# Kernel tuning notes

Hardware: AMD Instinct MI355X
Metric: run time of the kernel (lower is better)

Reference implementation:

```python
import jax, jax.numpy as jnp
import numpy as np
import math

D = 512      # d_model = sd_dim*2
DFF = 512    # dim_feedforward
S = 512      # num_seg (queries)
T = 32768    # video frames (keys)
RATE = 4     # self-attention band half-width
SCALE = 1.0 / math.sqrt(D)


def _ln(x, g, b):
    m = x.mean(-1, keepdims=True)
    v = ((x - m) ** 2).mean(-1, keepdims=True)
    return (x - m) / jnp.sqrt(v + 1e-5) * g + b


def setup_inputs() -> dict:
    key = jax.random.key(0)
    ks = jax.random.split(key, 12)
    w = lambda k, shp, s=0.02: jax.random.normal(k, shp, jnp.float32) * s
    # exactly S contiguous action segments over T frames
    action_idx = jnp.asarray((np.arange(T) * S) // T, dtype=jnp.int32)
    return dict(
        tgt=w(ks[0], (S, 1, D), 1.0), memory=w(ks[1], (T, 1, D), 1.0),
        pos=w(ks[2], (T, 1, D), 0.1), query_pos=w(ks[3], (S, 1, D), 0.1),
        action_idx=action_idx,
        ca_t2l_w=w(ks[4], (D, D)), ca_t2l_b=jnp.zeros(D),
        ca_l1_w=w(ks[5], (DFF, D)), ca_l1_b=jnp.zeros(DFF),
        ca_l2_w=w(ks[6], (D, DFF)), ca_l2_b=jnp.zeros(D),
        ca_n2_g=jnp.ones(D), ca_n2_b=jnp.zeros(D),
        ca_n3_g=jnp.ones(D), ca_n3_b=jnp.zeros(D),
        sa_conv_w=w(ks[7], (D, D)), sa_conv_b=jnp.zeros(D),
        sa_l1_w=w(ks[8], (DFF, D)), sa_l1_b=jnp.zeros(DFF),
        sa_l2_w=w(ks[9], (D, DFF)), sa_l2_b=jnp.zeros(D),
        sa_n1_g=jnp.ones(D), sa_n1_b=jnp.zeros(D),
        sa_n2_g=jnp.ones(D), sa_n2_b=jnp.zeros(D),
    )


def reference(tgt, memory, pos, query_pos, action_idx,
              ca_t2l_w, ca_t2l_b, ca_l1_w, ca_l1_b, ca_l2_w, ca_l2_b,
              ca_n2_g, ca_n2_b, ca_n3_g, ca_n3_b,
              sa_conv_w, sa_conv_b, sa_l1_w, sa_l1_b, sa_l2_w, sa_l2_b,
              sa_n1_g, sa_n1_b, sa_n2_g, sa_n2_b):
    # ---------------- CrossAttention (segment mask) ----------------
    q = tgt + query_pos                      # (S,1,D)
    k = memory + pos                         # (T,1,D)
    scores = jnp.einsum('sbd,tbd->bst', q, k) * SCALE   # (1,S,T)
    # segment id per frame from change points of action_idx
    chg = (action_idx[1:] != action_idx[:-1]).astype(jnp.int32)
    seg_id = jnp.concatenate([jnp.zeros(1, jnp.int32), jnp.cumsum(chg)])  # (T,)
    # query i attends to segments i-1, i, i+1
    mask = jnp.abs(seg_id[None, :] - jnp.arange(S, dtype=jnp.int32)[:, None]) <= 1  # (S,T)
    scores = jnp.where(mask[None], scores, -jnp.inf)
    attn = jax.nn.softmax(scores, axis=-1)               # (1,S,T)
    tgt2 = jnp.einsum('bst,tbd->sbd', attn, memory)      # (S,1,D)
    tgt2 = jnp.maximum(tgt2, 0.0) @ ca_t2l_w.T + ca_t2l_b
    x = _ln(tgt + tgt2, ca_n2_g, ca_n2_b)
    ffn = jnp.maximum(x @ ca_l1_w.T + ca_l1_b, 0.0) @ ca_l2_w.T + ca_l2_b
    x = _ln(x + ffn, ca_n3_g, ca_n3_b)                   # (S,1,D)
    # ---------------- SelfAttention (banded, pos=None) ----------------
    src = jnp.transpose(x, (1, 0, 2))                    # (1,S,D)
    s2 = jnp.einsum('bsd,btd->bst', src, src) * SCALE    # (1,S,S)
    i = jnp.arange(S)
    band = jnp.abs(i[:, None] - i[None, :]) <= RATE      # (S,S)
    s2 = jnp.where(band[None], s2, -jnp.inf)
    a2 = jax.nn.softmax(s2, axis=-1)                     # (1,S,S)
    src2 = jnp.einsum('bqk,bkd->bqd', a2, src)           # (1,S,D)
    src2 = jnp.maximum(src2, 0.0) @ sa_conv_w.T + sa_conv_b  # 1x1 conv over channels
    y = _ln(src + src2, sa_n1_g, sa_n1_b)
    ffn2 = jnp.maximum(y @ sa_l1_w.T + sa_l1_b, 0.0) @ sa_l2_w.T + sa_l2_b
    y = _ln(y + ffn2, sa_n2_g, sa_n2_b)
    return y                                              # (1,S,D)
```

## Files before the change

kernel.cpp:

```cpp
#include <hip/hip_runtime.h>

#define S_Q 512
#define DIM 512
#define SCALE_F 0.04419417382415922f
#define LDS_W 520

typedef short short8 __attribute__((ext_vector_type(8)));
typedef float floatx4 __attribute__((ext_vector_type(4)));

__device__ __forceinline__ float wave_sum(float v) {
#pragma unroll
  for (int o = 32; o > 0; o >>= 1) v += __shfl_xor(v, o);
  return v;
}
__device__ __forceinline__ unsigned short f2bf(float f) {
  unsigned u = __float_as_uint(f);
  return (unsigned short)((u + 0x7FFFu + ((u >> 16) & 1u)) >> 16);
}
__device__ __forceinline__ float bf2f(short s) {
  return __uint_as_float(((unsigned)(unsigned short)s) << 16);
}

__global__ __launch_bounds__(256) void k_ca_partial(
    const float* __restrict__ tgt, const float* __restrict__ qpos,
    const float* __restrict__ mem, const float* __restrict__ pos,
    unsigned short* __restrict__ part_acc, float* __restrict__ part_ms) {
  const int j = blockIdx.x;
  const int tid = threadIdx.x;
  const int wave = tid >> 6, lane = tid & 63;
  const int d0 = lane * 8;
  __shared__ float wacc[4][3][DIM];
  __shared__ float wms[4][3][2];

  float qf[3][8];
#pragma unroll
  for (int c = 0; c < 3; ++c) {
    const int qi = j - 1 + c;
    if ((unsigned)qi < (unsigned)S_Q) {
      float4 t0 = *(const float4*)(tgt + (size_t)qi * DIM + d0);
      float4 t1 = *(const float4*)(tgt + (size_t)qi * DIM + d0 + 4);
      float4 q0 = *(const float4*)(qpos + (size_t)qi * DIM + d0);
      float4 q1 = *(const float4*)(qpos + (size_t)qi * DIM + d0 + 4);
      qf[c][0] = t0.x + q0.x; qf[c][1] = t0.y + q0.y;
      qf[c][2] = t0.z + q0.z; qf[c][3] = t0.w + q0.w;
      qf[c][4] = t1.x + q1.x; qf[c][5] = t1.y + q1.y;
      qf[c][6] = t1.z + q1.z; qf[c][7] = t1.w + q1.w;
    } else {
#pragma unroll
      for (int e = 0; e < 8; ++e) qf[c][e] = 0.f;
    }
  }

  float m[3] = {-1e30f, -1e30f, -1e30f};
  float ssum[3] = {0.f, 0.f, 0.f};
  float acc[3][8];
#pragma unroll
  for (int c = 0; c < 3; ++c)
#pragma unroll
    for (int e = 0; e < 8; ++e) acc[c][e] = 0.f;

  const float* mbase = mem + ((size_t)j * 64 + wave * 16) * DIM + d0;
  const float* pbase = pos + ((size_t)j * 64 + wave * 16) * DIM + d0;

  for (int b = 0; b < 4; ++b) {
    float mv[4][8], kk[4][8];
#pragma unroll
    for (int f = 0; f < 4; ++f) {
      const float* mp = mbase + (size_t)(b * 4 + f) * DIM;
      const float* pp = pbase + (size_t)(b * 4 + f) * DIM;
      float4 a = *(const float4*)mp;
      float4 bb = *(const float4*)(mp + 4);
      float4 c4 = *(const float4*)pp;
      float4 dd = *(const float4*)(pp + 4);
      mv[f][0] = a.x;  mv[f][1] = a.y;  mv[f][2] = a.z;  mv[f][3] = a.w;
      mv[f][4] = bb.x; mv[f][5] = bb.y; mv[f][6] = bb.z; mv[f][7] = bb.w;
      kk[f][0] = a.x + c4.x;  kk[f][1] = a.y + c4.y;
      kk[f][2] = a.z + c4.z;  kk[f][3] = a.w + c4.w;
      kk[f][4] = bb.x + dd.x; kk[f][5] = bb.y + dd.y;
      kk[f][6] = bb.z + dd.z; kk[f][7] = bb.w + dd.w;
    }
    float dots[3][4];
#pragma unroll
    for (int f = 0; f < 4; ++f) {
      float s0 = 0.f, s1 = 0.f, s2 = 0.f;
#pragma unroll
      for (int e = 0; e < 8; ++e) {
        s0 += qf[0][e] * kk[f][e];
        s1 += qf[1][e] * kk[f][e];
        s2 += qf[2][e] * kk[f][e];
      }
      dots[0][f] = s0; dots[1][f] = s1; dots[2][f] = s2;
    }
#pragma unroll
    for (int o = 32; o > 0; o >>= 1)
#pragma unroll
      for (int c = 0; c < 3; ++c)
#pragma unroll
        for (int f = 0; f < 4; ++f) dots[c][f] += __shfl_xor(dots[c][f], o);
#pragma unroll
    for (int c = 0; c < 3; ++c) {
      float s[4];
#pragma unroll
      for (int f = 0; f < 4; ++f) s[f] = dots[c][f] * SCALE_F;
      const float bm = fmaxf(fmaxf(s[0], s[1]), fmaxf(s[2], s[3]));
      const float nm = fmaxf(m[c], bm);
      const float fct = __expf(m[c] - nm);
      m[c] = nm;
      ssum[c] *= fct;
#pragma unroll
      for (int e = 0; e < 8; ++e) acc[c][e] *= fct;
#pragma unroll
      for (int f = 0; f < 4; ++f) {
        const float w = __expf(s[f] - nm);
        ssum[c] += w;
#pragma unroll
        for (int e = 0; e < 8; ++e) acc[c][e] += w * mv[f][e];
      }
    }
  }

#pragma unroll
  for (int c = 0; c < 3; ++c) {
    *(float4*)(&wacc[wave][c][d0]) =
        make_float4(acc[c][0], acc[c][1], acc[c][2], acc[c][3]);
    *(float4*)(&wacc[wave][c][d0 + 4]) =
        make_float4(acc[c][4], acc[c][5], acc[c][6], acc[c][7]);
    if (lane == 0) { wms[wave][c][0] = m[c]; wms[wave][c][1] = ssum[c]; }
  }
  __syncthreads();

  const int d = tid * 2;
#pragma unroll
  for (int c = 0; c < 3; ++c) {
    const int qi = j - 1 + c;
    if ((unsigned)qi >= (unsigned)S_Q) continue;
    float M = wms[0][c][0];
#pragma unroll
    for (int w = 1; w < 4; ++w) M = fmaxf(M, wms[w][c][0]);
    float S = 0.f, ax = 0.f, ay = 0.f;
#pragma unroll
    for (int w = 0; w < 4; ++w) {
      const float wg = __expf(wms[w][c][0] - M);
      S += wg * wms[w][c][1];
      const float2 a = *(const float2*)(&wacc[w][c][d]);
      ax += wg * a.x;
      ay += wg * a.y;
    }
    const size_t slot = (size_t)qi * 3 + c;
    unsigned short* dst = part_acc + slot * DIM + d;
    dst[0] = f2bf(ax);
    dst[1] = f2bf(ay);
    if (tid == 0) {
      part_ms[slot * 2 + 0] = M;
      part_ms[slot * 2 + 1] = S;
    }
  }
}

__device__ __forceinline__ void stage_tile(const float* __restrict__ G,
                                           short* __restrict__ Ls,
                                           int rowblk, int tid) {
  const int w = tid >> 6, lane = tid & 63;
  const int col = lane * 8;
#pragma unroll
  for (int u = 0; u < 8; ++u) {
    const int row = u * 4 + w;
    const float* src = G + (size_t)(rowblk * 32 + row) * DIM + col;
    float4 a = *(const float4*)src;
    float4 b = *(const float4*)(src + 4);
    short8 s;
    s[0] = (short)f2bf(a.x); s[1] = (short)f2bf(a.y);
    s[2] = (short)f2bf(a.z); s[3] = (short)f2bf(a.w);
    s[4] = (short)f2bf(b.x); s[5] = (short)f2bf(b.y);
    s[6] = (short)f2bf(b.z); s[7] = (short)f2bf(b.w);
    *(short8*)(&Ls[row * LDS_W + col]) = s;
  }
}

template <bool RELU>
__device__ __forceinline__ void gemm_core(const short* __restrict__ As,
                                          const short* __restrict__ Ws,
                                          const float* __restrict__ bias,
                                          float* __restrict__ C, int bx, int by,
                                          int wave, int lane) {
  const int r0 = (wave >> 1) * 16, c0 = (wave & 1) * 16;
  const int frow = lane & 15, fk = (lane >> 4) * 8;
  const short* ap = &As[(r0 + frow) * LDS_W + fk];
  const short* wp = &Ws[(c0 + frow) * LDS_W + fk];
  floatx4 acc = {0.f, 0.f, 0.f, 0.f};
#pragma unroll
  for (int kc = 0; kc < 16; ++kc) {
    const short8 af = *(const short8*)(ap + kc * 32);
    const short8 wf = *(const short8*)(wp + kc * 32);
    acc = __builtin_amdgcn_mfma_f32_16x16x32_bf16(af, wf, acc, 0, 0, 0);
  }
  const int col = bx * 32 + c0 + frow;
  const int rowb = by * 32 + r0 + (lane >> 4) * 4;
  const float b = bias[col];
#pragma unroll
  for (int r = 0; r < 4; ++r) {
    float v = acc[r] + b;
    if (RELU) v = fmaxf(v, 0.f);
    C[(size_t)(rowb + r) * DIM + col] = v;
  }
}

__device__ __forceinline__ void ln_prologue(const float* __restrict__ X,
                                            const float* __restrict__ R,
                                            const float* __restrict__ g,
                                            const float* __restrict__ b,
                                            short* __restrict__ As, int by,
                                            float* x_out, int wave, int lane) {
  const int d0 = lane * 8;
  float gg[8], bb[8];
  {
    float4 g0 = *(const float4*)(g + d0);
    float4 g1 = *(const float4*)(g + d0 + 4);
    float4 b0 = *(const float4*)(b + d0);
    float4 b1 = *(const float4*)(b + d0 + 4);
    gg[0] = g0.x; gg[1] = g0.y; gg[2] = g0.z; gg[3] = g0.w;
    gg[4] = g1.x; gg[5] = g1.y; gg[6] = g1.z; gg[7] = g1.w;
    bb[0] = b0.x; bb[1] = b0.y; bb[2] = b0.z; bb[3] = b0.w;
    bb[4] = b1.x; bb[5] = b1.y; bb[6] = b1.z; bb[7] = b1.w;
  }
  for (int r = wave; r < 32; r += 4) {
    const int grow = by * 32 + r;
    const float* xp = X + (size_t)grow * DIM + d0;
    const float* rp = R + (size_t)grow * DIM + d0;
    float4 x0 = *(const float4*)xp;
    float4 x1 = *(const float4*)(xp + 4);
    float4 r0 = *(const float4*)rp;
    float4 r1 = *(const float4*)(rp + 4);
    float v[8] = {x0.x + r0.x, x0.y + r0.y, x0.z + r0.z, x0.w + r0.w,
                  x1.x + r1.x, x1.y + r1.y, x1.z + r1.z, x1.w + r1.w};
    float s = 0.f, sq = 0.f;
#pragma unroll
    for (int e = 0; e < 8; ++e) { s += v[e]; sq += v[e] * v[e]; }
#pragma unroll
    for (int o = 32; o > 0; o >>= 1) {
      s += __shfl_xor(s, o);
      sq += __shfl_xor(sq, o);
    }
    const float mean = s * (1.f / DIM);
    const float var = sq * (1.f / DIM) - mean * mean;
    const float rstd = rsqrtf(var + 1e-5f);
    float o8[8];
    short8 sv;
#pragma unroll
    for (int e = 0; e < 8; ++e) {
      o8[e] = (v[e] - mean) * rstd * gg[e] + bb[e];
      sv[e] = (short)f2bf(o8[e]);
    }
    *(short8*)(&As[r * LDS_W + d0]) = sv;
    if (x_out) {
      *(float4*)(x_out + (size_t)grow * DIM + d0) =
          make_float4(o8[0], o8[1], o8[2], o8[3]);
      *(float4*)(x_out + (size_t)grow * DIM + d0 + 4) =
          make_float4(o8[4], o8[5], o8[6], o8[7]);
    }
  }
}

__global__ __launch_bounds__(256) void k_g1(
    const unsigned short* __restrict__ part_acc,
    const float* __restrict__ part_ms, const float* __restrict__ W,
    const float* __restrict__ bias, float* __restrict__ C) {
  __shared__ short As[32 * LDS_W];
  __shared__ short Ws[32 * LDS_W];
  const int tid = threadIdx.x;
  const int bx = blockIdx.x, by = blockIdx.y;
  const int wave = tid >> 6, lane = tid & 63;
  const int d0 = lane * 8;
  for (int r = wave; r < 32; r += 4) {
    const int i = by * 32 + r;
    const bool valid[3] = {i < S_Q - 1, true, i > 0};
    float mm[3], ss[3], M = -1e30f;
#pragma unroll
    for (int c = 0; c < 3; ++c) {
      if (valid[c]) {
        mm[c] = part_ms[((size_t)i * 3 + c) * 2 + 0];
        ss[c] = part_ms[((size_t)i * 3 + c) * 2 + 1];
        M = fmaxf(M, mm[c]);
      } else {
        mm[c] = -1e30f;
        ss[c] = 0.f;
      }
    }
    float den = 0.f, wg[3];
#pragma unroll
    for (int c = 0; c < 3; ++c) {
      wg[c] = valid[c] ? __expf(mm[c] - M) : 0.f;
      den += wg[c] * ss[c];
    }
    const float inv = 1.f / den;
    float o[8] = {0.f, 0.f, 0.f, 0.f, 0.f, 0.f, 0.f, 0.f};
#pragma unroll
    for (int c = 0; c < 3; ++c) {
      if (valid[c]) {
        const short8 pa =
            *(const short8*)(part_acc + ((size_t)i * 3 + c) * DIM + d0);
#pragma unroll
        for (int e = 0; e < 8; ++e) o[e] += wg[c] * bf2f(pa[e]);
      }
    }
    short8 sv;
#pragma unroll
    for (int e = 0; e < 8; ++e) sv[e] = (short)f2bf(fmaxf(o[e] * inv, 0.f));
    *(short8*)(&As[r * LDS_W + d0]) = sv;
  }
  stage_tile(W, Ws, bx, tid);
  __syncthreads();
  gemm_core<false>(As, Ws, bias, C, bx, by, wave, lane);
}

__global__ __launch_bounds__(256) void k_gln(
    const float* __restrict__ X, const float* __restrict__ R,
    const float* __restrict__ g, const float* __restrict__ b,
    const float* __restrict__ W, const float* __restrict__ bias,
    float* __restrict__ C, float* __restrict__ x_out) {
  __shared__ short As[32 * LDS_W];
  __shared__ short Ws[32 * LDS_W];
  const int tid = threadIdx.x;
  const int bx = blockIdx.x, by = blockIdx.y;
  const int wave = tid >> 6, lane = tid & 63;
  ln_prologue(X, R, g, b, As, by, (bx == 0) ? x_out : nullptr, wave, lane);
  stage_tile(W, Ws, bx, tid);
  __syncthreads();
  gemm_core<true>(As, Ws, bias, C, bx, by, wave, lane);
}

__global__ __launch_bounds__(256) void k_gplain(
    const float* __restrict__ A, const float* __restrict__ W,
    const float* __restrict__ bias, float* __restrict__ C) {
  __shared__ short As[32 * LDS_W];
  __shared__ short Ws[32 * LDS_W];
  const int tid = threadIdx.x;
  const int bx = blockIdx.x, by = blockIdx.y;
  const int wave = tid >> 6, lane = tid & 63;
  stage_tile(A, As, by, tid);
  stage_tile(W, Ws, bx, tid);
  __syncthreads();
  gemm_core<false>(As, Ws, bias, C, bx, by, wave, lane);
}

__global__ __launch_bounds__(256) void k_g4(
    const float* __restrict__ X, const float* __restrict__ R,
    const float* __restrict__ g, const float* __restrict__ b,
    const float* __restrict__ W, const float* __restrict__ bias,
    float* __restrict__ C, float* __restrict__ x2_out) {
  __shared__ short Xw[40 * LDS_W];
  __shared__ short As[32 * LDS_W];
  __shared__ short Ws[32 * LDS_W];
  const int tid = threadIdx.x;
  const int bx = blockIdx.x, by = blockIdx.y;
  const int wave = tid >> 6, lane = tid & 63;
  const int d0 = lane * 8;
  const int wlo = (by * 32 - 4 > 0) ? by * 32 - 4 : 0;
  const int whi = (by * 32 + 35 < S_Q - 1) ? by * 32 + 35 : S_Q - 1;
  const int nw = whi - wlo + 1;

  {
    float gg[8], bb[8];
    float4 g0 = *(const float4*)(g + d0);
    float4 g1 = *(const float4*)(g + d0 + 4);
    float4 b0 = *(const float4*)(b + d0);
    float4 b1 = *(const float4*)(b + d0 + 4);
    gg[0] = g0.x; gg[1] = g0.y; gg[2] = g0.z; gg[3] = g0.w;
    gg[4] = g1.x; gg[5] = g1.y; gg[6] = g1.z; gg[7] = g1.w;
    bb[0] = b0.x; bb[1] = b0.y; bb[2] = b0.z; bb[3] = b0.w;
    bb[4] = b1.x; bb[5] = b1.y; bb[6] = b1.z; bb[7] = b1.w;
    for (int r = wave; r < nw; r += 4) {
      const int grow = wlo + r;
      const float* xp = X + (size_t)grow * DIM + d0;
      const float* rp = R + (size_t)grow * DIM + d0;
      float4 x0 = *(const float4*)xp;
      float4 x1 = *(const float4*)(xp + 4);
      float4 r0 = *(const float4*)rp;
      float4 r1 = *(const float4*)(rp + 4);
      float v[8] = {x0.x + r0.x, x0.y + r0.y, x0.z + r0.z, x0.w + r0.w,
                    x1.x + r1.x, x1.y + r1.y, x1.z + r1.z, x1.w + r1.w};
      float s = 0.f, sq = 0.f;
#pragma unroll
      for (int e = 0; e < 8; ++e) { s += v[e]; sq += v[e] * v[e]; }
#pragma unroll
      for (int o = 32; o > 0; o >>= 1) {
        s += __shfl_xor(s, o);
        sq += __shfl_xor(sq, o);
      }
      const float mean = s * (1.f / DIM);
      const float var = sq * (1.f / DIM) - mean * mean;
      const float rstd = rsqrtf(var + 1e-5f);
      float o8[8];
      short8 sv;
#pragma unroll
      for (int e = 0; e < 8; ++e) {
        o8[e] = (v[e] - mean) * rstd * gg[e] + bb[e];
        sv[e] = (short)f2bf(o8[e]);
      }
      *(short8*)(&Xw[r * LDS_W + d0]) = sv;
      if (bx == 0 && grow >= by * 32 && grow < by * 32 + 32) {
        *(float4*)(x2_out + (size_t)grow * DIM + d0) =
            make_float4(o8[0], o8[1], o8[2], o8[3]);
        *(float4*)(x2_out + (size_t)grow * DIM + d0 + 4) =
            make_float4(o8[4], o8[5], o8[6], o8[7]);
      }
    }
  }
  stage_tile(W, Ws, bx, tid);
  __syncthreads();

  for (int li = wave; li < 32; li += 4) {
    const int i = by * 32 + li;
    const int lq = i - wlo;
    float qv[8];
    {
      const short8 qs = *(const short8*)(&Xw[lq * LDS_W + d0]);
#pragma unroll
      for (int e = 0; e < 8; ++e) qv[e] = bf2f(qs[e]);
    }
    const int jlo = (i - 4 > 0) ? i - 4 : 0;
    const int jhi = (i + 4 < S_Q - 1) ? i + 4 : S_Q - 1;
    const int n = jhi - jlo + 1;
    float sc[9];
#pragma unroll
    for (int k = 0; k < 9; ++k) {
      if (k < n) {
        const int lk = jlo + k - wlo;
        const short8 ks = *(const short8*)(&Xw[lk * LDS_W + d0]);
        float dd = 0.f;
#pragma unroll
        for (int e = 0; e < 8; ++e) dd += qv[e] * bf2f(ks[e]);
        sc[k] = dd;
      } else {
        sc[k] = 0.f;
      }
    }
#pragma unroll
    for (int o = 32; o > 0; o >>= 1)
#pragma unroll
      for (int k = 0; k < 9; ++k) sc[k] += __shfl_xor(sc[k], o);
    float M = -1e30f;
#pragma unroll
    for (int k = 0; k < 9; ++k) {
      sc[k] *= SCALE_F;
      if (k < n) M = fmaxf(M, sc[k]);
    }
    float p[9], den = 0.f;
#pragma unroll
    for (int k = 0; k < 9; ++k) {
      p[k] = (k < n) ? __expf(sc[k] - M) : 0.f;
      den += p[k];
    }
    const float inv = 1.f / den;
    float o8[8] = {0.f, 0.f, 0.f, 0.f, 0.f, 0.f, 0.f, 0.f};
#pragma unroll
    for (int k = 0; k < 9; ++k) {
      if (k < n) {
        const int lk = jlo + k - wlo;
        const short8 ks = *(const short8*)(&Xw[lk * LDS_W + d0]);
#pragma unroll
        for (int e = 0; e < 8; ++e) o8[e] += p[k] * bf2f(ks[e]);
      }
    }
    short8 sv;
#pragma unroll
    for (int e = 0; e < 8; ++e) sv[e] = (short)f2bf(fmaxf(o8[e] * inv, 0.f));
    *(short8*)(&As[li * LDS_W + d0]) = sv;
  }
  __syncthreads();
  gemm_core<false>(As, Ws, bias, C, bx, by, wave, lane);
}

__global__ __launch_bounds__(256) void k_addln(
    const float* __restrict__ X, const float* __restrict__ R,
    const float* __restrict__ g, const float* __restrict__ b,
    float* __restrict__ out) {
  const int row = blockIdx.x * 4 + (threadIdx.x >> 6);
  const int lane = threadIdx.x & 63;
  const int d = lane * 8;
  const float4* xp = (const float4*)(X + (size_t)row * DIM + d);
  const float4* rp = (const float4*)(R + (size_t)row * DIM + d);
  float4 x0 = xp[0], x1 = xp[1], r0 = rp[0], r1 = rp[1];
  float v[8] = {x0.x + r0.x, x0.y + r0.y, x0.z + r0.z, x0.w + r0.w,
                x1.x + r1.x, x1.y + r1.y, x1.z + r1.z, x1.w + r1.w};
  float s = 0.f, sq = 0.f;
#pragma unroll
  for (int e = 0; e < 8; ++e) { s += v[e]; sq += v[e] * v[e]; }
  s = wave_sum(s);
  sq = wave_sum(sq);
  const float mean = s * (1.f / DIM);
  const float var = sq * (1.f / DIM) - mean * mean;
  const float rstd = rsqrtf(var + 1e-5f);
  const float4* gp = (const float4*)(g + d);
  const float4* bp = (const float4*)(b + d);
  float4 g0 = gp[0], g1 = gp[1], bb0 = bp[0], bb1 = bp[1];
  float4 o0, o1;
  o0.x = (v[0] - mean) * rstd * g0.x + bb0.x;
  o0.y = (v[1] - mean) * rstd * g0.y + bb0.y;
  o0.z = (v[2] - mean) * rstd * g0.z + bb0.z;
  o0.w = (v[3] - mean) * rstd * g0.w + bb0.w;
  o1.x = (v[4] - mean) * rstd * g1.x + bb1.x;
  o1.y = (v[5] - mean) * rstd * g1.y + bb1.y;
  o1.z = (v[6] - mean) * rstd * g1.z + bb1.z;
  o1.w = (v[7] - mean) * rstd * g1.w + bb1.w;
  *(float4*)(out + (size_t)row * DIM + d) = o0;
  *(float4*)(out + (size_t)row * DIM + d + 4) = o1;
}

extern "C" void kernel_launch(void* const* d_in, const int* in_sizes, int n_in,
                              void* d_out, int out_size, void* d_ws, size_t ws_size,
                              hipStream_t stream) {
  const float* tgt       = (const float*)d_in[0];
  const float* memory    = (const float*)d_in[1];
  const float* pos       = (const float*)d_in[2];
  const float* qpos      = (const float*)d_in[3];
  const float* ca_t2l_w  = (const float*)d_in[5];
  const float* ca_t2l_b  = (const float*)d_in[6];
  const float* ca_l1_w   = (const float*)d_in[7];
  const float* ca_l1_b   = (const float*)d_in[8];
  const float* ca_l2_w   = (const float*)d_in[9];
  const float* ca_l2_b   = (const float*)d_in[10];
  const float* ca_n2_g   = (const float*)d_in[11];
  const float* ca_n2_b   = (const float*)d_in[12];
  const float* ca_n3_g   = (const float*)d_in[13];
  const float* ca_n3_b   = (const float*)d_in[14];
  const float* sa_conv_w = (const float*)d_in[15];
  const float* sa_conv_b = (const float*)d_in[16];
  const float* sa_l1_w   = (const float*)d_in[17];
  const float* sa_l1_b   = (const float*)d_in[18];
  const float* sa_l2_w   = (const float*)d_in[19];
  const float* sa_l2_b   = (const float*)d_in[20];
  const float* sa_n1_g   = (const float*)d_in[21];
  const float* sa_n1_b   = (const float*)d_in[22];
  const float* sa_n2_g   = (const float*)d_in[23];
  const float* sa_n2_b   = (const float*)d_in[24];
  float* out = (float*)d_out;
  float* ws = (float*)d_ws;

  unsigned short* part_acc = (unsigned short*)ws;
  float* part_ms = ws + 393216;
  float* t2 = ws + 396288;
  float* h  = ws + 658432;
  float* x  = ws + 920576;
  float* f  = ws + 0;
  float* x2 = ws + 396288;
  float* c  = ws + 658432;
  float* y1 = ws + 0;
  float* h2 = ws + 920576;
  float* f2 = ws + 396288;

  const dim3 gg(16, 16, 1);

  k_ca_partial<<<512, 256, 0, stream>>>(tgt, qpos, memory, pos, part_acc, part_ms);
  k_g1<<<gg, 256, 0, stream>>>(part_acc, part_ms, ca_t2l_w, ca_t2l_b, t2);
  k_gln<<<gg, 256, 0, stream>>>(tgt, t2, ca_n2_g, ca_n2_b, ca_l1_w, ca_l1_b, h, x);
  k_gplain<<<gg, 256, 0, stream>>>(h, ca_l2_w, ca_l2_b, f);
  k_g4<<<gg, 256, 0, stream>>>(x, f, ca_n3_g, ca_n3_b, sa_conv_w, sa_conv_b, c, x2);
  k_gln<<<gg, 256, 0, stream>>>(x2, c, sa_n1_g, sa_n1_b, sa_l1_w, sa_l1_b, h2, y1);
  k_gplain<<<gg, 256, 0, stream>>>(h2, sa_l2_w, sa_l2_b, f2);
  k_addln<<<128, 256, 0, stream>>>(f2, y1, sa_n2_g, sa_n2_b, out);
}
```

Baseline: 282.1 us.

## Compute cross-attention scores with split-bf16 MFMA instead of shuffle reductions

The per-segment score computation moves from scalar FMA dot products with wave-wide shuffle reductions to MFMA 16x16x32 bf16 instructions. It uses a hi/lo bf16 split with three MFMAs to keep near-fp32 accuracy. Probabilities are staged in LDS and the weighted sum over memory runs as a second pass, which drops the online-softmax rescaling. The cost is that each wave reads mem twice (once for keys, once for values) and does extra bf16 conversion work. The partial-result store is also packed into a single 32-bit write.

Measured after the change: 287.0 us. No clear change (+1.7%).

```diff
diff --git a/kernel.cpp b/kernel.cpp
--- a/kernel.cpp
+++ b/kernel.cpp
@@ -27,105 +27,118 @@
     unsigned short* __restrict__ part_acc, float* __restrict__ part_ms) {
   const int j = blockIdx.x;
   const int tid = threadIdx.x;
-  const int wave = tid >> 6, lane = tid & 63;
-  const int d0 = lane * 8;
+  const int w = tid >> 6, lane = tid & 63;
+  __shared__ short q_hi[4][LDS_W];
+  __shared__ short q_lo[4][LDS_W];
+  __shared__ float p_lds[4][3][16];
   __shared__ float wacc[4][3][DIM];
   __shared__ float wms[4][3][2];
 
-  float qf[3][8];
-#pragma unroll
-  for (int c = 0; c < 3; ++c) {
-    const int qi = j - 1 + c;
-    if ((unsigned)qi < (unsigned)S_Q) {
+  {
+    const int d0 = lane * 8;
+    const int qi = j - 1 + w;
+    if (w < 3 && (unsigned)qi < (unsigned)S_Q) {
       float4 t0 = *(const float4*)(tgt + (size_t)qi * DIM + d0);
       float4 t1 = *(const float4*)(tgt + (size_t)qi * DIM + d0 + 4);
       float4 q0 = *(const float4*)(qpos + (size_t)qi * DIM + d0);
       float4 q1 = *(const float4*)(qpos + (size_t)qi * DIM + d0 + 4);
-      qf[c][0] = t0.x + q0.x; qf[c][1] = t0.y + q0.y;
-      qf[c][2] = t0.z + q0.z; qf[c][3] = t0.w + q0.w;
-      qf[c][4] = t1.x + q1.x; qf[c][5] = t1.y + q1.y;
-      qf[c][6] = t1.z + q1.z; qf[c][7] = t1.w + q1.w;
+      float v[8] = {t0.x + q0.x, t0.y + q0.y, t0.z + q0.z, t0.w + q0.w,
+                    t1.x + q1.x, t1.y + q1.y, t1.z + q1.z, t1.w + q1.w};
+      short8 hi, lo;
+#pragma unroll
+      for (int e = 0; e < 8; ++e) {
+        unsigned short h = f2bf(v[e]);
+        hi[e] = (short)h;
+        lo[e] = (short)f2bf(v[e] - bf2f((short)h));
+      }
+      *(short8*)(&q_hi[w][d0]) = hi;
+      *(short8*)(&q_lo[w][d0]) = lo;
     } else {
-#pragma unroll
-      for (int e = 0; e < 8; ++e) qf[c][e] = 0.f;
-    }
-  }
-
-  float m[3] = {-1e30f, -1e30f, -1e30f};
-  float ssum[3] = {0.f, 0.f, 0.f};
+      short8 z = {0, 0, 0, 0, 0, 0, 0, 0};
+      *(short8*)(&q_hi[w][d0]) = z;
+      *(short8*)(&q_lo[w][d0]) = z;
+    }
+  }
+  __syncthreads();
+
+  const int arow = lane & 15;
+  const int kgrp = lane >> 4;
+  const int qrow = (arow < 3) ? arow : 3;
+  const size_t rowoff = ((size_t)j * 64 + w * 16 + arow) * DIM;
+  floatx4 accS = {0.f, 0.f, 0.f, 0.f};
+#pragma unroll 4
+  for (int kc = 0; kc < 16; ++kc) {
+    const int col = kc * 32 + kgrp * 8;
+    float4 a0 = *(const float4*)(mem + rowoff + col);
+    float4 a1 = *(const float4*)(mem + rowoff + col + 4);
+    float4 p0 = *(const float4*)(pos + rowoff + col);
+    float4 p1 = *(const float4*)(pos + rowoff + col + 4);
+    float kv[8] = {a0.x + p0.x, a0.y + p0.y, a0.z + p0.z, a0.w + p0.w,
+                   a1.x + p1.x, a1.y + p1.y, a1.z + p1.z, a1.w + p1.w};
+    short8 ah, al;
+#pragma unroll
+    for (int e = 0; e < 8; ++e) {
+      unsigned short h = f2bf(kv[e]);
+      ah[e] = (short)h;
+      al[e] = (short)f2bf(kv[e] - bf2f((short)h));
+    }
+    const short8 qh = *(const short8*)(&q_hi[qrow][col]);
+    const short8 ql = *(const short8*)(&q_lo[qrow][col]);
+    accS = __builtin_amdgcn_mfma_f32_16x16x32_bf16(ah, qh, accS, 0, 0, 0);
+    accS = __builtin_amdgcn_mfma_f32_16x16x32_bf16(al, qh, accS, 0, 0, 0);
+    accS = __builtin_amdgcn_mfma_f32_16x16x32_bf16(ah, ql, accS, 0, 0, 0);
+  }
+  float s[4];
+#pragma unroll
+  for (int r = 0; r < 4; ++r) s[r] = accS[r] * SCALE_F;
+  float mloc = fmaxf(fmaxf(s[0], s[1]), fmaxf(s[2], s[3]));
+  mloc = fmaxf(mloc, __shfl_xor(mloc, 16));
+  mloc = fmaxf(mloc, __shfl_xor(mloc, 32));
+  float p[4], sloc = 0.f;
+#pragma unroll
+  for (int r = 0; r < 4; ++r) {
+    p[r] = __expf(s[r] - mloc);
+    sloc += p[r];
+  }
+  sloc += __shfl_xor(sloc, 16);
+  sloc += __shfl_xor(sloc, 32);
+  if (arow < 3) {
+    *(float4*)(&p_lds[w][arow][kgrp * 4]) = make_float4(p[0], p[1], p[2], p[3]);
+    if (lane < 3) {
+      wms[w][lane][0] = mloc;
+      wms[w][lane][1] = sloc;
+    }
+  }
+
+  const int d0 = lane * 8;
   float acc[3][8];
 #pragma unroll
   for (int c = 0; c < 3; ++c)
 #pragma unroll
     for (int e = 0; e < 8; ++e) acc[c][e] = 0.f;
-
-  const float* mbase = mem + ((size_t)j * 64 + wave * 16) * DIM + d0;
-  const float* pbase = pos + ((size_t)j * 64 + wave * 16) * DIM + d0;
-
-  for (int b = 0; b < 4; ++b) {
-    float mv[4][8], kk[4][8];
-#pragma unroll
-    for (int f = 0; f < 4; ++f) {
-      const float* mp = mbase + (size_t)(b * 4 + f) * DIM;
-      const float* pp = pbase + (size_t)(b * 4 + f) * DIM;
-      float4 a = *(const float4*)mp;
-      float4 bb = *(const float4*)(mp + 4);
-      float4 c4 = *(const float4*)pp;
-      float4 dd = *(const float4*)(pp + 4);
-      mv[f][0] = a.x;  mv[f][1] = a.y;  mv[f][2] = a.z;  mv[f][3] = a.w;
-      mv[f][4] = bb.x; mv[f][5] = bb.y; mv[f][6] = bb.z; mv[f][7] = bb.w;
-      kk[f][0] = a.x + c4.x;  kk[f][1] = a.y + c4.y;
-      kk[f][2] = a.z + c4.z;  kk[f][3] = a.w + c4.w;
-      kk[f][4] = bb.x + dd.x; kk[f][5] = bb.y + dd.y;
-      kk[f][6] = bb.z + dd.z; kk[f][7] = bb.w + dd.w;
-    }
-    float dots[3][4];
-#pragma unroll
-    for (int f = 0; f < 4; ++f) {
-      float s0 = 0.f, s1 = 0.f, s2 = 0.f;
-#pragma unroll
-      for (int e = 0; e < 8; ++e) {
-        s0 += qf[0][e] * kk[f][e];
-        s1 += qf[1][e] * kk[f][e];
-        s2 += qf[2][e] * kk[f][e];
-      }
-      dots[0][f] = s0; dots[1][f] = s1; dots[2][f] = s2;
-    }
-#pragma unroll
-    for (int o = 32; o > 0; o >>= 1)
-#pragma unroll
-      for (int c = 0; c < 3; ++c)
-#pragma unroll
-        for (int f = 0; f < 4; ++f) dots[c][f] += __shfl_xor(dots[c][f], o);
-#pragma unroll
-    for (int c = 0; c < 3; ++c) {
-      float s[4];
-#pragma unroll
-      for (int f = 0; f < 4; ++f) s[f] = dots[c][f] * SCALE_F;
-      const float bm = fmaxf(fmaxf(s[0], s[1]), fmaxf(s[2], s[3]));
-      const float nm = fmaxf(m[c], bm);
-      const float fct = __expf(m[c] - nm);
-      m[c] = nm;
-      ssum[c] *= fct;
-#pragma unroll
-      for (int e = 0; e < 8; ++e) acc[c][e] *= fct;
-#pragma unroll
-      for (int f = 0; f < 4; ++f) {
-        const float w = __expf(s[f] - nm);
-        ssum[c] += w;
-#pragma unroll
-        for (int e = 0; e < 8; ++e) acc[c][e] += w * mv[f][e];
-      }
+  const float* mb = mem + ((size_t)j * 64 + w * 16) * DIM + d0;
+#pragma unroll 4
+  for (int f = 0; f < 16; ++f) {
+    float4 m0 = *(const float4*)(mb + (size_t)f * DIM);
+    float4 m1 = *(const float4*)(mb + (size_t)f * DIM + 4);
+    const float mv[8] = {m0.x, m0.y, m0.z, m0.w, m1.x, m1.y, m1.z, m1.w};
+    const float w0 = p_lds[w][0][f];
+    const float w1 = p_lds[w][1][f];
+    const float w2 = p_lds[w][2][f];
+#pragma unroll
+    for (int e = 0; e < 8; ++e) {
+      acc[0][e] += w0 * mv[e];
+      acc[1][e] += w1 * mv[e];
+      acc[2][e] += w2 * mv[e];
     }
   }
 
 #pragma unroll
   for (int c = 0; c < 3; ++c) {
-    *(float4*)(&wacc[wave][c][d0]) =
+    *(float4*)(&wacc[w][c][d0]) =
         make_float4(acc[c][0], acc[c][1], acc[c][2], acc[c][3]);
-    *(float4*)(&wacc[wave][c][d0 + 4]) =
+    *(float4*)(&wacc[w][c][d0 + 4]) =
         make_float4(acc[c][4], acc[c][5], acc[c][6], acc[c][7]);
-    if (lane == 0) { wms[wave][c][0] = m[c]; wms[wave][c][1] = ssum[c]; }
   }
   __syncthreads();
 
@@ -136,20 +149,19 @@
     if ((unsigned)qi >= (unsigned)S_Q) continue;
     float M = wms[0][c][0];
 #pragma unroll
-    for (int w = 1; w < 4; ++w) M = fmaxf(M, wms[w][c][0]);
+    for (int u = 1; u < 4; ++u) M = fmaxf(M, wms[u][c][0]);
     float S = 0.f, ax = 0.f, ay = 0.f;
 #pragma unroll
-    for (int w = 0; w < 4; ++w) {
-      const float wg = __expf(wms[w][c][0] - M);
-      S += wg * wms[w][c][1];
-      const float2 a = *(const float2*)(&wacc[w][c][d]);
+    for (int u = 0; u < 4; ++u) {
+      const float wg = __expf(wms[u][c][0] - M);
+      S += wg * wms[u][c][1];
+      const float2 a = *(const float2*)(&wacc[u][c][d]);
       ax += wg * a.x;
       ay += wg * a.y;
     }
     const size_t slot = (size_t)qi * 3 + c;
-    unsigned short* dst = part_acc + slot * DIM + d;
-    dst[0] = f2bf(ax);
-    dst[1] = f2bf(ay);
+    unsigned* dst = (unsigned*)(part_acc + slot * DIM + d);
+    *dst = (unsigned)f2bf(ax) | ((unsigned)f2bf(ay) << 16);
     if (tid == 0) {
       part_ms[slot * 2 + 0] = M;
       part_ms[slot * 2 + 1] = S;
```
